# Optimization experiments

Measured on AMD Instinct MI355X. Metric: run time of the kernel, lower is better.

Reference implementation:

```python
import jax, jax.numpy as jnp
import numpy as np

B, H = 1024, 1024
HID, RHID = 128, 64
DT = 1.0
EPS = 1e-6
SCALES = np.array([0.01, 0.02, 2000.0, 5.0], dtype=np.float32)  # R0[ohm], R1[ohm], C1[F], Q[Ah]


def analytic_ocv(soc):
    # smooth analytic open-circuit-voltage curve (Li-ion-like)
    return 3.0 + 1.2 * soc - 0.5 * soc * soc + 0.3 * soc * soc * soc


def setup_inputs() -> dict:
    key = jax.random.key(0)
    ks = jax.random.split(key, 12)
    inp = {
        "V": jax.random.normal(ks[0], (B, H), jnp.float32),
        "I": jax.random.normal(ks[1], (B, H), jnp.float32),
        "Tz": jax.random.normal(ks[2], (B, H), jnp.float32),
        "soc0": jax.random.uniform(ks[3], (B,), jnp.float32),
        # ParamHead: (soc, I, T) -> 4 positive ECM params
        "W1p": jax.random.normal(ks[4], (3, HID), jnp.float32) / np.sqrt(3.0),
        "b1p": jnp.zeros((HID,), jnp.float32),
        "W2p": jax.random.normal(ks[5], (HID, 4), jnp.float32) / np.sqrt(HID),
        "b2p": jnp.zeros((4,), jnp.float32),
        # ResidualNN: (soc, I, T) -> scalar voltage correction
        "W1r": jax.random.normal(ks[6], (3, RHID), jnp.float32) / np.sqrt(3.0),
        "b1r": jnp.zeros((RHID,), jnp.float32),
        "W2r": jax.random.normal(ks[7], (RHID, 1), jnp.float32) / np.sqrt(RHID),
        "b2r": jnp.zeros((1,), jnp.float32),
    }
    return inp


def _rollout(I, Tz, soc0, W1p, b1p, W2p, b2p, W1r, b1r, W2r, b2r):
    scales = jnp.asarray(SCALES)

    def step(carry, inp_t):
        soc, v1 = carry                       # (B,), (B,)
        I_t, T_t = inp_t                      # (B,), (B,)
        feats = jnp.stack([soc, I_t, T_t], axis=-1)  # (B,3)
        # ParamHead MLP -> positive params via softplus*scale + eps
        hp = jnp.tanh(feats @ W1p + b1p)
        params = jax.nn.softplus(hp @ W2p + b2p) * scales + EPS  # (B,4)
        R0, R1, C1, Q = params[:, 0], params[:, 1], params[:, 2], params[:, 3]
        # ResidualNN correction
        hr = jnp.tanh(feats @ W1r + b1r)
        resid = (hr @ W2r + b2r)[:, 0]        # (B,)
        # Euler ODE updates: RC polarization branch + coulomb counting
        v1_new = v1 + DT * (-v1 / (R1 * C1) + I_t / C1)
        soc_new = jnp.clip(soc - DT * I_t / (Q * 3600.0), 0.0, 1.0)
        V_pred = analytic_ocv(soc_new) - I_t * R0 - v1_new + resid
        return (soc_new, v1_new), V_pred

    carry0 = (soc0, jnp.zeros_like(soc0))
    xs = (I.T, Tz.T)                          # time-major (H,B)
    _, V_pred = jax.lax.scan(step, carry0, xs)
    return V_pred.T                           # (B,H)


def reference(V, I, Tz, soc0, W1p, b1p, W2p, b2p, W1r, b1r, W2r, b2r):
    soc0 = jnp.where(jnp.isnan(soc0), 0.8, soc0)  # default soc0=0.8 semantics
    return _rollout(I, Tz, soc0, W1p, b1p, W2p, b2p, W1r, b1r, W2r, b2r)
```

## Files before the change

### kernel.cpp

```cpp
#include <hip/hip_runtime.h>


#define NB 1024
#define HT 1024
#define HIDN 128
#define NCHUNK 16

#define K2  2.885390081777927f
#define KL  1.4426950408889634f
#define LN2 0.6931471805599453f

typedef unsigned uint2v __attribute__((ext_vector_type(2)));

__device__ __forceinline__ float readlane_f(float v, int lane) {
    int r = __builtin_amdgcn_readlane(__builtin_bit_cast(int, v), lane);
    return __builtin_bit_cast(float, r);
}

template <int CTRL, int RMASK>
__device__ __forceinline__ float dpp_add(float x) {
    int s = __builtin_amdgcn_update_dpp(0, __builtin_bit_cast(int, x),
                                        CTRL, RMASK, 0xF, true);
    return x + __builtin_bit_cast(float, s);
}

__device__ __forceinline__ void permlane32_swap(float& a, float& b) {
    uint2v r = __builtin_amdgcn_permlane32_swap(
        __builtin_bit_cast(unsigned, a), __builtin_bit_cast(unsigned, b),
        false, false);
    a = __builtin_bit_cast(float, r[0]);
    b = __builtin_bit_cast(float, r[1]);
}

__device__ __forceinline__ float swz_xor16(float x) {
    int r = __builtin_amdgcn_ds_swizzle(__builtin_bit_cast(int, x), 0x401F);
    return __builtin_bit_cast(float, r);
}

__device__ __forceinline__ float tanh_ps(float z) {
    float t = __builtin_amdgcn_exp2f(z);
    float r = __builtin_amdgcn_rcpf(t + 1.0f);
    return fmaf(-2.0f, r, 1.0f);
}

__global__ __launch_bounds__(128, 1) void rollout_kernel(
    const float* __restrict__ Iin, const float* __restrict__ Tzin,
    const float* __restrict__ soc0,
    const float* __restrict__ W1p, const float* __restrict__ b1p,
    const float* __restrict__ W2p, const float* __restrict__ b2p,
    const float* __restrict__ W1r, const float* __restrict__ b1r,
    const float* __restrict__ W2r, const float* __restrict__ b2r,
    float* __restrict__ out)
{
    const int b    = blockIdx.x;
    const int wid  = threadIdx.x >> 6;
    const int lane = threadIdx.x & 63;

    __shared__ float4 handBuf[2][64];
    __shared__ float4 coefS[64];
    __shared__ float  w2rS[64];

    const float* Ib = Iin  + (size_t)b * HT;
    const float* Tb = Tzin + (size_t)b * HT;
    float*       Ob = out  + (size_t)b * HT;
    const float b2rr = b2r[0];

    float w1pa0=0,w1pa1=0,w1pa2=0,bpa=0, w1pb0=0,w1pb1=0,w1pb2=0,bpb=0;
    float w2pa0=0,w2pa1=0,w2pa2=0,w2pa3=0, w2pb0=0,w2pb1=0,w2pb2=0,w2pb3=0;
    float biasLane=0, scaleLane=0;
    float socv=0, v1=0, Inext=0, Tnext=0;
    const int row = lane >> 4;
    const bool oddrow = (row & 1) != 0;

    if (wid == 0) {
        const int ja = lane, jb = lane + 64;
        w1pa0 = W1p[0*HIDN+ja]*K2; w1pa1 = W1p[1*HIDN+ja]*K2; w1pa2 = W1p[2*HIDN+ja]*K2;
        w1pb0 = W1p[0*HIDN+jb]*K2; w1pb1 = W1p[1*HIDN+jb]*K2; w1pb2 = W1p[2*HIDN+jb]*K2;
        bpa = b1p[ja]*K2; bpb = b1p[jb]*K2;
        w2pa0 = W2p[ja*4+0]*KL; w2pa1 = W2p[ja*4+1]*KL;
        w2pa2 = W2p[ja*4+2]*KL; w2pa3 = W2p[ja*4+3]*KL;
        w2pb0 = W2p[jb*4+0]*KL; w2pb1 = W2p[jb*4+1]*KL;
        w2pb2 = W2p[jb*4+2]*KL; w2pb3 = W2p[jb*4+3]*KL;
        const float b2p0 = b2p[0], b2p1 = b2p[1], b2p2 = b2p[2], b2p3 = b2p[3];
        biasLane  = ((row == 0) ? b2p0 : (row == 1) ? b2p2 : (row == 2) ? b2p1 : b2p3) * KL;
        scaleLane = ((row == 0) ? 0.01f : (row == 1) ? 2000.0f : (row == 2) ? 0.02f : 5.0f) * LN2;

        socv = soc0[b];
        unsigned u = __builtin_bit_cast(unsigned, socv);
        if ((u & 0x7FFFFFFFu) > 0x7F800000u) socv = 0.8f;
        v1 = 0.0f;
        Inext = Ib[lane];
        Tnext = Tb[lane];
    }

    for (int c = 0; c <= NCHUNK; ++c) {
        if (wid == 0) {
            if (c < NCHUNK) {
                const float Ibuf = Inext;
                const float Tbuf = Tnext;
                const int t1 = (c + 1) * 64;
                if (t1 < HT) { Inext = Ib[t1 + lane]; Tnext = Tb[t1 + lane]; }

                float4 hand = make_float4(0.f, 0.f, 0.f, 0.f);
                #pragma unroll 4
                for (int s = 0; s < 64; ++s) {
                    const float It = readlane_f(Ibuf, s);
                    const float Tt = readlane_f(Tbuf, s);
                    const float carry = socv;

                    const float za = fmaf(Tt, w1pa2, fmaf(It, w1pa1, fmaf(socv, w1pa0, bpa)));
                    const float zb = fmaf(Tt, w1pb2, fmaf(It, w1pb1, fmaf(socv, w1pb0, bpb)));
                    const float ha = tanh_ps(za);
                    const float hb = tanh_ps(zb);

                    float p0 = fmaf(hb, w2pb0, ha * w2pa0);
                    float p1 = fmaf(hb, w2pb1, ha * w2pa1);
                    float p2 = fmaf(hb, w2pb2, ha * w2pa2);
                    float p3 = fmaf(hb, w2pb3, ha * w2pa3);

                    permlane32_swap(p0, p1); float ab = p0 + p1;
                    permlane32_swap(p2, p3); float cd = p2 + p3;
                    ab += swz_xor16(ab);
                    cd += swz_xor16(cd);
                    float z = oddrow ? cd : ab;
                    z = dpp_add<0x111, 0xF>(z);
                    z = dpp_add<0x112, 0xF>(z);
                    z = dpp_add<0x114, 0xF>(z);
                    z = dpp_add<0x118, 0xF>(z);

                    const float e   = __builtin_amdgcn_exp2f(z + biasLane);
                    const float lg  = __builtin_amdgcn_logf(e + 1.0f);
                    const float par = fmaf(lg, scaleLane, 1e-6f);
                    const float ipar = __builtin_amdgcn_rcpf(par);
                    const float R0    = readlane_f(par, 15);
                    const float invC1 = readlane_f(ipar, 31);
                    const float invR1 = readlane_f(ipar, 47);
                    const float invQ  = readlane_f(ipar, 63);

                    const float invR1C1 = invR1 * invC1;
                    v1 = v1 + fmaf(-v1, invR1C1, It * invC1);
                    socv = fmaf(It * invQ, -2.77777777777778e-4f, socv);
                    socv = __builtin_amdgcn_fmed3f(socv, 0.0f, 1.0f);

                    const bool m = (lane == s);
                    hand.x = m ? carry : hand.x;
                    hand.y = m ? socv  : hand.y;
                    hand.z = m ? v1    : hand.z;
                    hand.w = m ? R0    : hand.w;
                }
                handBuf[c & 1][lane] = hand;
            }
        } else {
            if (c == 0) {
                coefS[lane] = make_float4(W1r[0*64+lane]*K2, W1r[1*64+lane]*K2,
                                          W1r[2*64+lane]*K2, b1r[lane]*K2);
                w2rS[lane] = W2r[lane];
            } else {
                const int cc = c - 1;
                const float4 h  = handBuf[cc & 1][lane];
                const float  Is = Ib[cc * 64 + lane];
                const float  Ts = Tb[cc * 64 + lane];

                float acc = b2rr;
                #pragma unroll 8
                for (int j = 0; j < 64; ++j) {
                    const float4 w  = coefS[j];
                    const float  wr = w2rS[j];
                    const float z  = fmaf(Ts, w.z, fmaf(Is, w.y, fmaf(h.x, w.x, w.w)));
                    acc = fmaf(tanh_ps(z), wr, acc);
                }

                const float s1  = h.y;
                const float ocv = fmaf(s1, fmaf(s1, fmaf(s1, 0.3f, -0.5f), 1.2f), 3.0f);
                const float Vp  = (fmaf(-Is, h.w, ocv) - h.z) + acc;
                Ob[cc * 64 + lane] = Vp;
            }
        }
        __syncthreads();
    }
}

extern "C" void kernel_launch(void* const* d_in, const int* in_sizes, int n_in,
                              void* d_out, int out_size, void* d_ws, size_t ws_size,
                              hipStream_t stream) {
    const float* Iin  = (const float*)d_in[1];
    const float* Tzin = (const float*)d_in[2];
    const float* soc0 = (const float*)d_in[3];
    const float* W1p  = (const float*)d_in[4];
    const float* b1p  = (const float*)d_in[5];
    const float* W2p  = (const float*)d_in[6];
    const float* b2p  = (const float*)d_in[7];
    const float* W1r  = (const float*)d_in[8];
    const float* b1r  = (const float*)d_in[9];
    const float* W2r  = (const float*)d_in[10];
    const float* b2r  = (const float*)d_in[11];
    float* out = (float*)d_out;

    hipLaunchKernelGGL(rollout_kernel, dim3(NB), dim3(128), 0, stream,
                       Iin, Tzin, soc0, W1p, b1p, W2p, b2p, W1r, b1r, W2r, b2r, out);
}
```

Before: 276.6 us.

## Shrink serial SOC chain to Q-only; move R0/R1/C1 and v1 scan to consumer wave

The serial wave 0 loop now computes only the Q column of the parameter head, so it needs a single cross-lane reduction and no longer builds R0, R1, C1 or v1 on the critical dependency chain. Wave 1 recomputes the full 128-wide hidden layer per timestep to get R0, R1 and C1 in parallel across lanes. It then evaluates the linear v1 recurrence with a 64-lane Kogge-Stone affine scan, carrying v1 between chunks. This shortens the per-step latency of the sequential SOC recurrence but adds substantial parallel work to the consumer wave, which may now become the bottleneck. The scan's reassociation also changes rounding slightly.

```diff
diff --git a/kernel.cpp b/kernel.cpp
--- a/kernel.cpp
+++ b/kernel.cpp
@@ -9,8 +9,8 @@
 #define K2  2.885390081777927f
 #define KL  1.4426950408889634f
 #define LN2 0.6931471805599453f
-
-typedef unsigned uint2v __attribute__((ext_vector_type(2)));
+#define EPSP 1e-6f
+#define SOCK -2.77777777777778e-4f
 
 __device__ __forceinline__ float readlane_f(float v, int lane) {
     int r = __builtin_amdgcn_readlane(__builtin_bit_cast(int, v), lane);
@@ -22,19 +22,6 @@
     int s = __builtin_amdgcn_update_dpp(0, __builtin_bit_cast(int, x),
                                         CTRL, RMASK, 0xF, true);
     return x + __builtin_bit_cast(float, s);
-}
-
-__device__ __forceinline__ void permlane32_swap(float& a, float& b) {
-    uint2v r = __builtin_amdgcn_permlane32_swap(
-        __builtin_bit_cast(unsigned, a), __builtin_bit_cast(unsigned, b),
-        false, false);
-    a = __builtin_bit_cast(float, r[0]);
-    b = __builtin_bit_cast(float, r[1]);
-}
-
-__device__ __forceinline__ float swz_xor16(float x) {
-    int r = __builtin_amdgcn_ds_swizzle(__builtin_bit_cast(int, x), 0x401F);
-    return __builtin_bit_cast(float, r);
 }
 
 __device__ __forceinline__ float tanh_ps(float z) {
@@ -56,41 +43,39 @@
     const int wid  = threadIdx.x >> 6;
     const int lane = threadIdx.x & 63;
 
-    __shared__ float4 handBuf[2][64];
-    __shared__ float4 coefS[64];
+    __shared__ float2 handBuf[2][64];
+    __shared__ float4 pcoefS[128];
+    __shared__ float4 poutS[128];
+    __shared__ float4 rcoefS[64];
     __shared__ float  w2rS[64];
 
     const float* Ib = Iin  + (size_t)b * HT;
     const float* Tb = Tzin + (size_t)b * HT;
     float*       Ob = out  + (size_t)b * HT;
-    const float b2rr = b2r[0];
 
     float w1pa0=0,w1pa1=0,w1pa2=0,bpa=0, w1pb0=0,w1pb1=0,w1pb2=0,bpb=0;
-    float w2pa0=0,w2pa1=0,w2pa2=0,w2pa3=0, w2pb0=0,w2pb1=0,w2pb2=0,w2pb3=0;
-    float biasLane=0, scaleLane=0;
-    float socv=0, v1=0, Inext=0, Tnext=0;
-    const int row = lane >> 4;
-    const bool oddrow = (row & 1) != 0;
+    float w2pa3=0, w2pb3=0, biasQ=0;
+    float socv=0, Inext=0, Tnext=0;
+
+    float v1c = 0.0f;
+    float bias0=0, bias1=0, bias2=0, b2rr=0;
 
     if (wid == 0) {
         const int ja = lane, jb = lane + 64;
         w1pa0 = W1p[0*HIDN+ja]*K2; w1pa1 = W1p[1*HIDN+ja]*K2; w1pa2 = W1p[2*HIDN+ja]*K2;
         w1pb0 = W1p[0*HIDN+jb]*K2; w1pb1 = W1p[1*HIDN+jb]*K2; w1pb2 = W1p[2*HIDN+jb]*K2;
         bpa = b1p[ja]*K2; bpb = b1p[jb]*K2;
-        w2pa0 = W2p[ja*4+0]*KL; w2pa1 = W2p[ja*4+1]*KL;
-        w2pa2 = W2p[ja*4+2]*KL; w2pa3 = W2p[ja*4+3]*KL;
-        w2pb0 = W2p[jb*4+0]*KL; w2pb1 = W2p[jb*4+1]*KL;
-        w2pb2 = W2p[jb*4+2]*KL; w2pb3 = W2p[jb*4+3]*KL;
-        const float b2p0 = b2p[0], b2p1 = b2p[1], b2p2 = b2p[2], b2p3 = b2p[3];
-        biasLane  = ((row == 0) ? b2p0 : (row == 1) ? b2p2 : (row == 2) ? b2p1 : b2p3) * KL;
-        scaleLane = ((row == 0) ? 0.01f : (row == 1) ? 2000.0f : (row == 2) ? 0.02f : 5.0f) * LN2;
+        w2pa3 = W2p[ja*4+3]*KL; w2pb3 = W2p[jb*4+3]*KL;
+        biasQ = b2p[3]*KL;
 
         socv = soc0[b];
         unsigned u = __builtin_bit_cast(unsigned, socv);
         if ((u & 0x7FFFFFFFu) > 0x7F800000u) socv = 0.8f;
-        v1 = 0.0f;
         Inext = Ib[lane];
         Tnext = Tb[lane];
+    } else {
+        bias0 = b2p[0]*KL; bias1 = b2p[1]*KL; bias2 = b2p[2]*KL;
+        b2rr  = b2r[0];
     }
 
     for (int c = 0; c <= NCHUNK; ++c) {
@@ -101,78 +86,107 @@
                 const int t1 = (c + 1) * 64;
                 if (t1 < HT) { Inext = Ib[t1 + lane]; Tnext = Tb[t1 + lane]; }
 
-                float4 hand = make_float4(0.f, 0.f, 0.f, 0.f);
-                #pragma unroll 4
+                float2 hand = make_float2(0.f, 0.f);
+                #pragma unroll 8
                 for (int s = 0; s < 64; ++s) {
-                    const float It = readlane_f(Ibuf, s);
-                    const float Tt = readlane_f(Tbuf, s);
+                    const float It  = readlane_f(Ibuf, s);
+                    const float Tt  = readlane_f(Tbuf, s);
+                    const float ItK = It * SOCK;
+                    const float base_a = fmaf(Tt, w1pa2, fmaf(It, w1pa1, bpa));
+                    const float base_b = fmaf(Tt, w1pb2, fmaf(It, w1pb1, bpb));
                     const float carry = socv;
 
-                    const float za = fmaf(Tt, w1pa2, fmaf(It, w1pa1, fmaf(socv, w1pa0, bpa)));
-                    const float zb = fmaf(Tt, w1pb2, fmaf(It, w1pb1, fmaf(socv, w1pb0, bpb)));
-                    const float ha = tanh_ps(za);
-                    const float hb = tanh_ps(zb);
-
-                    float p0 = fmaf(hb, w2pb0, ha * w2pa0);
-                    float p1 = fmaf(hb, w2pb1, ha * w2pa1);
-                    float p2 = fmaf(hb, w2pb2, ha * w2pa2);
-                    float p3 = fmaf(hb, w2pb3, ha * w2pa3);
-
-                    permlane32_swap(p0, p1); float ab = p0 + p1;
-                    permlane32_swap(p2, p3); float cd = p2 + p3;
-                    ab += swz_xor16(ab);
-                    cd += swz_xor16(cd);
-                    float z = oddrow ? cd : ab;
+                    const float ha = tanh_ps(fmaf(socv, w1pa0, base_a));
+                    const float hb = tanh_ps(fmaf(socv, w1pb0, base_b));
+
+                    float z = fmaf(hb, w2pb3, ha * w2pa3);
                     z = dpp_add<0x111, 0xF>(z);
                     z = dpp_add<0x112, 0xF>(z);
                     z = dpp_add<0x114, 0xF>(z);
                     z = dpp_add<0x118, 0xF>(z);
-
-                    const float e   = __builtin_amdgcn_exp2f(z + biasLane);
-                    const float lg  = __builtin_amdgcn_logf(e + 1.0f);
-                    const float par = fmaf(lg, scaleLane, 1e-6f);
-                    const float ipar = __builtin_amdgcn_rcpf(par);
-                    const float R0    = readlane_f(par, 15);
-                    const float invC1 = readlane_f(ipar, 31);
-                    const float invR1 = readlane_f(ipar, 47);
-                    const float invQ  = readlane_f(ipar, 63);
-
-                    const float invR1C1 = invR1 * invC1;
-                    v1 = v1 + fmaf(-v1, invR1C1, It * invC1);
-                    socv = fmaf(It * invQ, -2.77777777777778e-4f, socv);
-                    socv = __builtin_amdgcn_fmed3f(socv, 0.0f, 1.0f);
+                    z = dpp_add<0x142, 0xA>(z);
+                    z = dpp_add<0x143, 0xC>(z);
+
+                    const float e  = __builtin_amdgcn_exp2f(z + biasQ);
+                    const float lg = __builtin_amdgcn_logf(e + 1.0f);
+                    const float Q  = fmaf(lg, 5.0f*LN2, EPSP);
+                    const float invQ = readlane_f(__builtin_amdgcn_rcpf(Q), 63);
+
+                    socv = __builtin_amdgcn_fmed3f(fmaf(ItK, invQ, socv), 0.0f, 1.0f);
 
                     const bool m = (lane == s);
                     hand.x = m ? carry : hand.x;
                     hand.y = m ? socv  : hand.y;
-                    hand.z = m ? v1    : hand.z;
-                    hand.w = m ? R0    : hand.w;
                 }
                 handBuf[c & 1][lane] = hand;
             }
         } else {
             if (c == 0) {
-                coefS[lane] = make_float4(W1r[0*64+lane]*K2, W1r[1*64+lane]*K2,
-                                          W1r[2*64+lane]*K2, b1r[lane]*K2);
+                pcoefS[lane]    = make_float4(W1p[0*HIDN+lane]*K2, W1p[1*HIDN+lane]*K2,
+                                              W1p[2*HIDN+lane]*K2, b1p[lane]*K2);
+                pcoefS[lane+64] = make_float4(W1p[0*HIDN+lane+64]*K2, W1p[1*HIDN+lane+64]*K2,
+                                              W1p[2*HIDN+lane+64]*K2, b1p[lane+64]*K2);
+                poutS[lane]     = make_float4(W2p[lane*4+0]*KL, W2p[lane*4+1]*KL,
+                                              W2p[lane*4+2]*KL, 0.f);
+                poutS[lane+64]  = make_float4(W2p[(lane+64)*4+0]*KL, W2p[(lane+64)*4+1]*KL,
+                                              W2p[(lane+64)*4+2]*KL, 0.f);
+                rcoefS[lane] = make_float4(W1r[0*64+lane]*K2, W1r[1*64+lane]*K2,
+                                           W1r[2*64+lane]*K2, b1r[lane]*K2);
                 w2rS[lane] = W2r[lane];
             } else {
                 const int cc = c - 1;
-                const float4 h  = handBuf[cc & 1][lane];
-                const float  Is = Ib[cc * 64 + lane];
-                const float  Ts = Tb[cc * 64 + lane];
+                const float2 h = handBuf[cc & 1][lane];
+                const float carry = h.x;
+                const float post  = h.y;
+                const float Is = Ib[cc * 64 + lane];
+                const float Ts = Tb[cc * 64 + lane];
+
+                float aR0 = bias0, aR1 = bias1, aC1 = bias2;
+                #pragma unroll 4
+                for (int j = 0; j < 128; ++j) {
+                    const float4 cj = pcoefS[j];
+                    const float4 oj = poutS[j];
+                    const float hj = tanh_ps(fmaf(Ts, cj.z, fmaf(Is, cj.y,
+                                             fmaf(carry, cj.x, cj.w))));
+                    aR0 = fmaf(hj, oj.x, aR0);
+                    aR1 = fmaf(hj, oj.y, aR1);
+                    aC1 = fmaf(hj, oj.z, aC1);
+                }
+                const float R0 = fmaf(__builtin_amdgcn_logf(
+                                      __builtin_amdgcn_exp2f(aR0) + 1.0f), 0.01f*LN2, EPSP);
+                const float R1 = fmaf(__builtin_amdgcn_logf(
+                                      __builtin_amdgcn_exp2f(aR1) + 1.0f), 0.02f*LN2, EPSP);
+                const float C1 = fmaf(__builtin_amdgcn_logf(
+                                      __builtin_amdgcn_exp2f(aC1) + 1.0f), 2000.0f*LN2, EPSP);
+                const float invC1   = __builtin_amdgcn_rcpf(C1);
+                const float invR1C1 = __builtin_amdgcn_rcpf(R1) * invC1;
+
+                float A_ = 1.0f - invR1C1;
+                float B_ = Is * invC1;
+                #pragma unroll
+                for (int d = 1; d < 64; d <<= 1) {
+                    float Au = __shfl_up(A_, d);
+                    float Bu = __shfl_up(B_, d);
+                    const bool ok = (lane >= d);
+                    Au = ok ? Au : 1.0f;
+                    Bu = ok ? Bu : 0.0f;
+                    const float Bn = fmaf(A_, Bu, B_);
+                    A_ = A_ * Au;
+                    B_ = Bn;
+                }
+                const float v1n = fmaf(A_, v1c, B_);
+                v1c = readlane_f(v1n, 63);
 
                 float acc = b2rr;
-                #pragma unroll 8
+                #pragma unroll 4
                 for (int j = 0; j < 64; ++j) {
-                    const float4 w  = coefS[j];
-                    const float  wr = w2rS[j];
-                    const float z  = fmaf(Ts, w.z, fmaf(Is, w.y, fmaf(h.x, w.x, w.w)));
-                    acc = fmaf(tanh_ps(z), wr, acc);
-                }
-
-                const float s1  = h.y;
-                const float ocv = fmaf(s1, fmaf(s1, fmaf(s1, 0.3f, -0.5f), 1.2f), 3.0f);
-                const float Vp  = (fmaf(-Is, h.w, ocv) - h.z) + acc;
+                    const float4 rj = rcoefS[j];
+                    acc = fmaf(tanh_ps(fmaf(Ts, rj.z, fmaf(Is, rj.y,
+                               fmaf(carry, rj.x, rj.w)))), w2rS[j], acc);
+                }
+
+                const float ocv = fmaf(post, fmaf(post, fmaf(post, 0.3f, -0.5f), 1.2f), 3.0f);
+                const float Vp  = (fmaf(-Is, R0, ocv) - v1n) + acc;
                 Ob[cc * 64 + lane] = Vp;
             }
         }
```

Measured after the change: 266.5 us. 3.7% less time.
